# Kernel optimization log

Hardware: AMD Instinct MI355X
Metric: run time of the kernel (lower is better)

The kernel has to match this reference:

```python
import jax, jax.numpy as jnp
import numpy as np

N, F_IN, H, MH = 50000, 128, 128, 256
E = 800000

def _lin_init(key, out_d, in_d, bias=True):
    k1, k2 = jax.random.split(key)
    bound = 1.0 / np.sqrt(in_d)
    W = jax.random.uniform(k1, (out_d, in_d), minval=-bound, maxval=bound, dtype=jnp.float32)
    if bias:
        b = jax.random.uniform(k2, (out_d,), minval=-bound, maxval=bound, dtype=jnp.float32)
        return W, b
    return W, None

def setup_inputs() -> dict:
    key = jax.random.key(0)
    ks = jax.random.split(key, 8)
    x = jax.random.normal(ks[0], (N, F_IN), dtype=jnp.float32)
    edge_index = jax.random.randint(ks[1], (2, E), 0, N, dtype=jnp.int64)
    W1l, b1l = _lin_init(ks[2], H, F_IN, bias=True)   # SAGEConv1 neighbor lin (with bias)
    W1r, _ = _lin_init(ks[3], H, F_IN, bias=False)    # SAGEConv1 root lin (no bias)
    W2l, b2l = _lin_init(ks[4], H, H, bias=True)
    W2r, _ = _lin_init(ks[5], H, H, bias=False)
    Wm1, bm1 = _lin_init(ks[6], MH, 2 * H, bias=True)
    Wm2, bm2 = _lin_init(ks[7], 1, MH, bias=True)
    return {"x": x, "edge_index": edge_index,
            "W1l": W1l, "b1l": b1l, "W1r": W1r,
            "W2l": W2l, "b2l": b2l, "W2r": W2r,
            "Wm1": Wm1, "bm1": bm1, "Wm2": Wm2, "bm2": bm2}

def _sage_conv(x, src, dst, Wl, bl, Wr, num_nodes):
    # mean-aggregate messages x[src] at dst, then lin_l(agg) + lin_r(x)
    agg = jax.ops.segment_sum(x[src], dst, num_segments=num_nodes)
    cnt = jax.ops.segment_sum(jnp.ones((src.shape[0],), x.dtype), dst, num_segments=num_nodes)
    agg = agg / jnp.maximum(cnt, 1.0)[:, None]
    return agg @ Wl.T + bl + x @ Wr.T

def reference(x, edge_index, W1l, b1l, W1r, W2l, b2l, W2r, Wm1, bm1, Wm2, bm2):
    src, dst = edge_index[0], edge_index[1]
    n = x.shape[0]
    h = jax.nn.relu(_sage_conv(x, src, dst, W1l, b1l, W1r, n))
    # dropout is identity in eval mode
    h = jax.nn.relu(_sage_conv(h, src, dst, W2l, b2l, W2r, n))
    ef = jnp.concatenate([h[src], h[dst]], axis=-1)  # [E, 2H]
    out = jax.nn.relu(ef @ Wm1.T + bm1) @ Wm2.T + bm2
    return out.reshape(-1)
```

## Files before the change

### kernel.cpp

```cpp
#include <hip/hip_runtime.h>
#include <hip/hip_bf16.h>

#define NN 50000
#define F 128
#define EE 800000
#define MHD 256

typedef __attribute__((ext_vector_type(8))) short bf16x8;
typedef __attribute__((ext_vector_type(4))) float f32x4;

__device__ __forceinline__ float b2f(unsigned short u) {
    union { unsigned int i; float f; } v; v.i = ((unsigned)u) << 16; return v.f;
}
__device__ __forceinline__ unsigned short f2b(float f) {
    unsigned int x = __float_as_uint(f);
    unsigned int r = x + 0x7fffu + ((x >> 16) & 1u);
    return (unsigned short)(r >> 16);
}

__global__ __launch_bounds__(256) void cast_zero_kernel(
    const float* __restrict__ x,
    const float* __restrict__ W1l, const float* __restrict__ W1r,
    const float* __restrict__ W2l, const float* __restrict__ W2r,
    const float* __restrict__ Wm1,
    unsigned short* __restrict__ xb, unsigned short* __restrict__ wb,
    int* __restrict__ deg) {
    int bid = blockIdx.x;
    if (bid < 6250) {
        int i = (bid * 256 + threadIdx.x) * 4;
        float4 v = *(const float4*)(x + i);
        ushort4 o; o.x = f2b(v.x); o.y = f2b(v.y); o.z = f2b(v.z); o.w = f2b(v.w);
        *(ushort4*)(xb + i) = o;
    } else if (bid < 6378) {
        int i = ((bid - 6250) * 256 + threadIdx.x) * 4;
        unsigned short o[4];
        if (i < 32768) {
            const float* p = (i < 16384) ? (W1l + i) : (W1r + (i - 16384));
            float4 v = *(const float4*)p;
            o[0] = f2b(v.x); o[1] = f2b(v.y); o[2] = f2b(v.z); o[3] = f2b(v.w);
        } else if (i < 65536) {
            int local = i - 32768;
            const float* M = (local < 16384) ? W2l : W2r;
            int lm = local & 16383;
            int n = lm >> 7, kp = lm & 127;
#pragma unroll
            for (int t = 0; t < 4; t++) {
                int k = ((kp + t) & 7) * 16 + ((kp + t) >> 3);
                o[t] = f2b(M[n * 128 + k]);
            }
        } else {
            int local = i - 65536;
            int n = local >> 8, k2 = local & 255;
            int half = k2 >> 7, kp = k2 & 127;
#pragma unroll
            for (int t = 0; t < 4; t++) {
                int k = half * 128 + ((kp + t) & 7) * 16 + ((kp + t) >> 3);
                o[t] = f2b(Wm1[n * 256 + k]);
            }
        }
        *(ushort4*)(wb + i) = *(ushort4*)o;
    } else {
        int idx = ((bid - 6378) * 256 + threadIdx.x) * 4;
        if (idx < 50016) *(int4*)(deg + idx) = (int4){0, 0, 0, 0};
    }
}

__global__ __launch_bounds__(256) void edge_cvt_hist_kernel(
    const int* __restrict__ ei, int* __restrict__ s32, int* __restrict__ d32,
    int* __restrict__ deg) {
    __shared__ int isI64;
    if (threadIdx.x == 0) {
        int z = 0;
        for (int i = 1; i < 128; i += 2) z |= ei[i];
        isI64 = (z == 0) ? 1 : 0;
    }
    __syncthreads();
    int e = blockIdx.x * 256 + threadIdx.x;
    if (e >= EE) return;
    int s, d;
    if (isI64) {
        const long long* e64 = (const long long*)ei;
        s = (int)e64[e];
        d = (int)e64[EE + e];
    } else {
        s = ei[e];
        d = ei[EE + e];
    }
    s32[e] = s;
    d32[e] = d;
    atomicAdd(&deg[d], 1);
}

__global__ __launch_bounds__(1024) void scan_p1_kernel(
    const int* __restrict__ deg, int* __restrict__ exloc, int* __restrict__ bsum) {
    __shared__ int part[1024];
    int t = threadIdx.x, gid = blockIdx.x * 1024 + t;
    int v = (gid < NN) ? deg[gid] : 0;
    part[t] = v;
    __syncthreads();
    for (int off = 1; off < 1024; off <<= 1) {
        int u = (t >= off) ? part[t - off] : 0;
        __syncthreads();
        part[t] += u;
        __syncthreads();
    }
    exloc[gid] = part[t] - v;
    if (t == 1023) bsum[blockIdx.x] = part[t];
}

__global__ __launch_bounds__(1024) void scan_p3_kernel(
    const int* __restrict__ exloc, const int* __restrict__ bsum,
    int* __restrict__ rowstart, int* __restrict__ cursor) {
    __shared__ int offs;
    if (threadIdx.x == 0) {
        int s = 0;
        for (int b = 0; b < blockIdx.x; b++) s += bsum[b];
        offs = s;
    }
    __syncthreads();
    int gid = blockIdx.x * 1024 + threadIdx.x;
    if (gid > NN) return;
    if (gid == NN) { rowstart[NN] = EE; return; }
    int r = exloc[gid] + offs;
    rowstart[gid] = r;
    cursor[gid] = r;
}

__global__ __launch_bounds__(256) void fill_kernel(
    const int* __restrict__ s32, const int* __restrict__ d32,
    int* __restrict__ cursor, int2* __restrict__ nedge) {
    int e = blockIdx.x * 256 + threadIdx.x;
    if (e < EE) {
        int p = atomicAdd(&cursor[d32[e]], 1);
        nedge[p] = make_int2(s32[e], e);
    }
}

__global__ __launch_bounds__(256) void sage_layer_kernel(
    const unsigned short* __restrict__ xin,
    const int2* __restrict__ nedge, const int* __restrict__ rowstart,
    const unsigned short* __restrict__ W1, const unsigned short* __restrict__ W2,
    const float* __restrict__ bias,
    unsigned short* __restrict__ out) {
    __shared__ unsigned short lds[4][16][136];
    int wave = threadIdx.x >> 6, lane = threadIdx.x & 63;
    int m0 = (blockIdx.x * 4 + wave) * 16;

    int g = lane >> 4, l16 = lane & 15, col8 = l16 * 8;
    for (int batch = 0; batch < 4; batch++) {
        int node = m0 + batch * 4 + g;
        int beg = 0, end = 0;
        if (node < NN) { beg = rowstart[node]; end = rowstart[node + 1]; }
        float a[8] = {0,0,0,0,0,0,0,0};
        float b[8] = {0,0,0,0,0,0,0,0};
        int j = beg;
        for (; j + 7 < end; j += 8) {
            int s0 = nedge[j].x,     s1 = nedge[j + 1].x, s2 = nedge[j + 2].x, s3 = nedge[j + 3].x;
            int s4 = nedge[j + 4].x, s5 = nedge[j + 5].x, s6 = nedge[j + 6].x, s7 = nedge[j + 7].x;
            bf16x8 v0 = *(const bf16x8*)(xin + (size_t)s0 * F + col8);
            bf16x8 v1 = *(const bf16x8*)(xin + (size_t)s1 * F + col8);
            bf16x8 v2 = *(const bf16x8*)(xin + (size_t)s2 * F + col8);
            bf16x8 v3 = *(const bf16x8*)(xin + (size_t)s3 * F + col8);
            bf16x8 v4 = *(const bf16x8*)(xin + (size_t)s4 * F + col8);
            bf16x8 v5 = *(const bf16x8*)(xin + (size_t)s5 * F + col8);
            bf16x8 v6 = *(const bf16x8*)(xin + (size_t)s6 * F + col8);
            bf16x8 v7 = *(const bf16x8*)(xin + (size_t)s7 * F + col8);
            for (int i = 0; i < 8; i++)
                a[i] += (b2f((unsigned short)v0[i]) + b2f((unsigned short)v1[i]))
                      + (b2f((unsigned short)v2[i]) + b2f((unsigned short)v3[i]));
            for (int i = 0; i < 8; i++)
                b[i] += (b2f((unsigned short)v4[i]) + b2f((unsigned short)v5[i]))
                      + (b2f((unsigned short)v6[i]) + b2f((unsigned short)v7[i]));
        }
        for (; j + 3 < end; j += 4) {
            int s0 = nedge[j].x, s1 = nedge[j + 1].x, s2 = nedge[j + 2].x, s3 = nedge[j + 3].x;
            bf16x8 v0 = *(const bf16x8*)(xin + (size_t)s0 * F + col8);
            bf16x8 v1 = *(const bf16x8*)(xin + (size_t)s1 * F + col8);
            bf16x8 v2 = *(const bf16x8*)(xin + (size_t)s2 * F + col8);
            bf16x8 v3 = *(const bf16x8*)(xin + (size_t)s3 * F + col8);
            for (int i = 0; i < 8; i++)
                a[i] += (b2f((unsigned short)v0[i]) + b2f((unsigned short)v1[i]))
                      + (b2f((unsigned short)v2[i]) + b2f((unsigned short)v3[i]));
        }
        for (; j < end; j++) {
            int s0 = nedge[j].x;
            bf16x8 v0 = *(const bf16x8*)(xin + (size_t)s0 * F + col8);
            for (int i = 0; i < 8; i++) a[i] += b2f((unsigned short)v0[i]);
        }
        float inv = 1.0f / fmaxf((float)(end - beg), 1.0f);
        unsigned short o[8];
        for (int i = 0; i < 8; i++) o[i] = f2b((a[i] + b[i]) * inv);
        *(bf16x8*)&lds[wave][batch * 4 + g][col8] = *(bf16x8*)o;
    }
    __syncthreads();

    int c = lane & 15, q = lane >> 4;
    f32x4 acc[8];
    for (int nt = 0; nt < 8; nt++) {
        float b = bias[nt * 16 + c];
        acc[nt] = (f32x4){b, b, b, b};
    }
    int mrow = m0 + c; if (mrow > NN - 1) mrow = NN - 1;
    for (int op = 0; op < 2; op++) {
        const unsigned short* W = op ? W2 : W1;
        for (int kb = 0; kb < 4; kb++) {
            bf16x8 a;
            if (op == 0) a = *(const bf16x8*)&lds[wave][c][kb * 32 + q * 8];
            else         a = *(const bf16x8*)(xin + (size_t)mrow * F + kb * 32 + q * 8);
            for (int nt = 0; nt < 8; nt++) {
                bf16x8 b = *(const bf16x8*)(W + (size_t)(nt * 16 + c) * F + kb * 32 + q * 8);
                acc[nt] = __builtin_amdgcn_mfma_f32_16x16x32_bf16(a, b, acc[nt], 0, 0, 0);
            }
        }
    }
#pragma unroll
    for (int r = 0; r < 4; r++) {
        int node = m0 + q * 4 + r;
        if (node < NN) {
            unsigned short o[8];
#pragma unroll
            for (int nt = 0; nt < 8; nt++) o[nt] = f2b(fmaxf(acc[nt][r], 0.0f));
            *(bf16x8*)(out + (size_t)node * F + c * 8) = *(bf16x8*)o;
        }
    }
}

__global__ __launch_bounds__(256) void pq_gemm_kernel(
    const unsigned short* __restrict__ h,
    const unsigned short* __restrict__ wmb,
    const float* __restrict__ bm1,
    unsigned short* __restrict__ PQ) {
    int wave = threadIdx.x >> 6, lane = threadIdx.x & 63;
    int c = lane & 15, q = lane >> 4;
    int half = wave >> 1, ntBase = (wave & 1) * 8;
    int m0 = blockIdx.x * 16;
    int mrow = m0 + c; if (mrow > NN - 1) mrow = NN - 1;
    bf16x8 a[4];
#pragma unroll
    for (int kb = 0; kb < 4; kb++)
        a[kb] = *(const bf16x8*)(h + (size_t)mrow * F + kb * 32 + q * 8);
    f32x4 acc[8];
#pragma unroll
    for (int nt = 0; nt < 8; nt++) {
        float b = half ? bm1[(ntBase + nt) * 16 + c] : 0.0f;
        acc[nt] = (f32x4){b, b, b, b};
    }
#pragma unroll
    for (int kb = 0; kb < 4; kb++) {
#pragma unroll
        for (int nt = 0; nt < 8; nt++) {
            bf16x8 b = *(const bf16x8*)(wmb + (size_t)((ntBase + nt) * 16 + c) * 256 + half * 128 + kb * 32 + q * 8);
            acc[nt] = __builtin_amdgcn_mfma_f32_16x16x32_bf16(a[kb], b, acc[nt], 0, 0, 0);
        }
    }
#pragma unroll
    for (int r = 0; r < 4; r++) {
        int node = m0 + q * 4 + r;
        if (node < NN) {
            unsigned short o[8];
#pragma unroll
            for (int nt = 0; nt < 8; nt++) o[nt] = f2b(acc[nt][r]);
            *(bf16x8*)(PQ + (size_t)node * 512 + half * 256 + c * 16 + ntBase) = *(bf16x8*)o;
        }
    }
}

__global__ __launch_bounds__(256) void edge_dot_kernel(
    const unsigned short* __restrict__ PQ,
    const int2* __restrict__ nedge, const int* __restrict__ rowstart,
    const float* __restrict__ Wm2, const float* __restrict__ bm2,
    float* __restrict__ out) {
    int wave = threadIdx.x >> 6, lane = threadIdx.x & 63;
    int node = blockIdx.x * 4 + wave;
    if (node >= NN) return;
    int g = lane >> 4, l16 = lane & 15;
    int col = l16 * 16;
    float w2f[16], qf[16];
#pragma unroll
    for (int i = 0; i < 16; i++) w2f[i] = Wm2[i * 16 + l16];
    {
        bf16x8 q0 = *(const bf16x8*)(PQ + (size_t)node * 512 + 256 + col);
        bf16x8 q1 = *(const bf16x8*)(PQ + (size_t)node * 512 + 256 + col + 8);
#pragma unroll
        for (int i = 0; i < 8; i++) { qf[i] = b2f((unsigned short)q0[i]); qf[8 + i] = b2f((unsigned short)q1[i]); }
    }
    float b2 = bm2[0];
    int beg = rowstart[node], end = rowstart[node + 1];
    int j = beg + g;
    for (; j + 4 < end; j += 8) {
        int2 e0 = nedge[j], e1 = nedge[j + 4];
        uint4 a0 = *(const uint4*)(PQ + (size_t)e0.x * 512 + col);
        uint4 a1 = *(const uint4*)(PQ + (size_t)e0.x * 512 + col + 8);
        uint4 c0 = *(const uint4*)(PQ + (size_t)e1.x * 512 + col);
        uint4 c1 = *(const uint4*)(PQ + (size_t)e1.x * 512 + col + 8);
        float t0 = 0.f, t1 = 0.f;
        unsigned int w0[8] = {a0.x, a0.y, a0.z, a0.w, a1.x, a1.y, a1.z, a1.w};
        unsigned int w1[8] = {c0.x, c0.y, c0.z, c0.w, c1.x, c1.y, c1.z, c1.w};
#pragma unroll
        for (int i = 0; i < 8; i++) {
            float lo0 = __uint_as_float(w0[i] << 16);
            float hi0 = __uint_as_float(w0[i] & 0xffff0000u);
            float lo1 = __uint_as_float(w1[i] << 16);
            float hi1 = __uint_as_float(w1[i] & 0xffff0000u);
            t0 += fmaxf(lo0 + qf[2 * i], 0.f) * w2f[2 * i]
                + fmaxf(hi0 + qf[2 * i + 1], 0.f) * w2f[2 * i + 1];
            t1 += fmaxf(lo1 + qf[2 * i], 0.f) * w2f[2 * i]
                + fmaxf(hi1 + qf[2 * i + 1], 0.f) * w2f[2 * i + 1];
        }
        t0 += __shfl_xor(t0, 1);  t1 += __shfl_xor(t1, 1);
        t0 += __shfl_xor(t0, 2);  t1 += __shfl_xor(t1, 2);
        t0 += __shfl_xor(t0, 4);  t1 += __shfl_xor(t1, 4);
        t0 += __shfl_xor(t0, 8);  t1 += __shfl_xor(t1, 8);
        if (l16 == 0) { out[e0.y] = t0 + b2; out[e1.y] = t1 + b2; }
    }
    for (; j < end; j += 4) {
        int2 e0 = nedge[j];
        uint4 a0 = *(const uint4*)(PQ + (size_t)e0.x * 512 + col);
        uint4 a1 = *(const uint4*)(PQ + (size_t)e0.x * 512 + col + 8);
        unsigned int w0[8] = {a0.x, a0.y, a0.z, a0.w, a1.x, a1.y, a1.z, a1.w};
        float t = 0.f;
#pragma unroll
        for (int i = 0; i < 8; i++) {
            float lo = __uint_as_float(w0[i] << 16);
            float hi = __uint_as_float(w0[i] & 0xffff0000u);
            t += fmaxf(lo + qf[2 * i], 0.f) * w2f[2 * i]
               + fmaxf(hi + qf[2 * i + 1], 0.f) * w2f[2 * i + 1];
        }
        t += __shfl_xor(t, 1);
        t += __shfl_xor(t, 2);
        t += __shfl_xor(t, 4);
        t += __shfl_xor(t, 8);
        if (l16 == 0) out[e0.y] = t + b2;
    }
}

extern "C" void kernel_launch(void* const* d_in, const int* in_sizes, int n_in,
                              void* d_out, int out_size, void* d_ws, size_t ws_size,
                              hipStream_t stream) {
    const float* x   = (const float*)d_in[0];
    const int*   ei  = (const int*)d_in[1];
    const float* W1l = (const float*)d_in[2];
    const float* b1l = (const float*)d_in[3];
    const float* W1r = (const float*)d_in[4];
    const float* W2l = (const float*)d_in[5];
    const float* b2l = (const float*)d_in[6];
    const float* W2r = (const float*)d_in[7];
    const float* Wm1 = (const float*)d_in[8];
    const float* bm1 = (const float*)d_in[9];
    const float* Wm2 = (const float*)d_in[10];
    const float* bm2 = (const float*)d_in[11];

    char* ws = (char*)d_ws;
    unsigned short* PQ       = (unsigned short*)(ws);
    unsigned short* xb       = (unsigned short*)(ws);
    unsigned short* h1       = (unsigned short*)(ws + 12800000);
    unsigned short* wb       = (unsigned short*)(ws + 51200000);
    int*            s32      = (int*)(ws + 51462144);
    int*            d32      = (int*)(ws + 54662144);
    int*            deg      = (int*)(ws + 57862144);
    int*            rowstart = (int*)(ws + 58062208);
    int*            cursor   = (int*)(ws + 58262272);
    int2*           nedge    = (int2*)(ws + 58462336);
    unsigned short* h2       = (unsigned short*)(ws + 64862336);
    int*            exloc    = (int*)(ws + 77662336);
    int*            bsum     = (int*)(ws + 77867136);
    float*          outp     = (float*)d_out;

    const unsigned short* w1l_b  = wb;
    const unsigned short* w1r_b  = wb + 16384;
    const unsigned short* w2l_p  = wb + 32768;
    const unsigned short* w2r_p  = wb + 49152;
    const unsigned short* wm1_p  = wb + 65536;

    cast_zero_kernel<<<6427, 256, 0, stream>>>(x, W1l, W1r, W2l, W2r, Wm1, xb, wb, deg);
    edge_cvt_hist_kernel<<<3125, 256, 0, stream>>>(ei, s32, d32, deg);
    scan_p1_kernel<<<50, 1024, 0, stream>>>(deg, exloc, bsum);
    scan_p3_kernel<<<50, 1024, 0, stream>>>(exloc, bsum, rowstart, cursor);
    fill_kernel<<<3125, 256, 0, stream>>>(s32, d32, cursor, nedge);

    sage_layer_kernel<<<782, 256, 0, stream>>>(xb, nedge, rowstart, w1l_b, w1r_b, b1l, h1);
    sage_layer_kernel<<<782, 256, 0, stream>>>(h1, nedge, rowstart, w2l_p, w2r_p, b2l, h2);
    pq_gemm_kernel<<<3125, 256, 0, stream>>>(h2, wm1_p, bm1, PQ);
    edge_dot_kernel<<<12500, 256, 0, stream>>>(PQ, nedge, rowstart, Wm2, bm2, outp);
}
```

Before: 427.3 us.

## Make edge MLP kernel edge-parallel with packed src/dst indices

```diff
diff --git a/kernel.cpp b/kernel.cpp
--- a/kernel.cpp
+++ b/kernel.cpp
@@ -22,9 +22,9 @@
     const float* __restrict__ x,
     const float* __restrict__ W1l, const float* __restrict__ W1r,
     const float* __restrict__ W2l, const float* __restrict__ W2r,
-    const float* __restrict__ Wm1,
+    const float* __restrict__ Wm1, const float* __restrict__ Wm2,
     unsigned short* __restrict__ xb, unsigned short* __restrict__ wb,
-    int* __restrict__ deg) {
+    int* __restrict__ deg, float* __restrict__ w2p) {
     int bid = blockIdx.x;
     if (bid < 6250) {
         int i = (bid * 256 + threadIdx.x) * 4;
@@ -59,9 +59,12 @@
             }
         }
         *(ushort4*)(wb + i) = *(ushort4*)o;
-    } else {
+    } else if (bid < 6427) {
         int idx = ((bid - 6378) * 256 + threadIdx.x) * 4;
         if (idx < 50016) *(int4*)(deg + idx) = (int4){0, 0, 0, 0};
+    } else {
+        int t = threadIdx.x;
+        w2p[t] = Wm2[(t & 15) * 16 + (t >> 4)];
     }
 }
 
@@ -131,8 +134,9 @@
     int* __restrict__ cursor, int2* __restrict__ nedge) {
     int e = blockIdx.x * 256 + threadIdx.x;
     if (e < EE) {
-        int p = atomicAdd(&cursor[d32[e]], 1);
-        nedge[p] = make_int2(s32[e], e);
+        int d = d32[e];
+        int p = atomicAdd(&cursor[d], 1);
+        nedge[p] = make_int2((int)((unsigned)s32[e] | ((unsigned)d << 16)), e);
     }
 }
 
@@ -155,8 +159,10 @@
         float b[8] = {0,0,0,0,0,0,0,0};
         int j = beg;
         for (; j + 7 < end; j += 8) {
-            int s0 = nedge[j].x,     s1 = nedge[j + 1].x, s2 = nedge[j + 2].x, s3 = nedge[j + 3].x;
-            int s4 = nedge[j + 4].x, s5 = nedge[j + 5].x, s6 = nedge[j + 6].x, s7 = nedge[j + 7].x;
+            int s0 = nedge[j].x & 0xffff,     s1 = nedge[j + 1].x & 0xffff;
+            int s2 = nedge[j + 2].x & 0xffff, s3 = nedge[j + 3].x & 0xffff;
+            int s4 = nedge[j + 4].x & 0xffff, s5 = nedge[j + 5].x & 0xffff;
+            int s6 = nedge[j + 6].x & 0xffff, s7 = nedge[j + 7].x & 0xffff;
             bf16x8 v0 = *(const bf16x8*)(xin + (size_t)s0 * F + col8);
             bf16x8 v1 = *(const bf16x8*)(xin + (size_t)s1 * F + col8);
             bf16x8 v2 = *(const bf16x8*)(xin + (size_t)s2 * F + col8);
@@ -173,7 +179,8 @@
                       + (b2f((unsigned short)v6[i]) + b2f((unsigned short)v7[i]));
         }
         for (; j + 3 < end; j += 4) {
-            int s0 = nedge[j].x, s1 = nedge[j + 1].x, s2 = nedge[j + 2].x, s3 = nedge[j + 3].x;
+            int s0 = nedge[j].x & 0xffff,     s1 = nedge[j + 1].x & 0xffff;
+            int s2 = nedge[j + 2].x & 0xffff, s3 = nedge[j + 3].x & 0xffff;
             bf16x8 v0 = *(const bf16x8*)(xin + (size_t)s0 * F + col8);
             bf16x8 v1 = *(const bf16x8*)(xin + (size_t)s1 * F + col8);
             bf16x8 v2 = *(const bf16x8*)(xin + (size_t)s2 * F + col8);
@@ -183,7 +190,7 @@
                       + (b2f((unsigned short)v2[i]) + b2f((unsigned short)v3[i]));
         }
         for (; j < end; j++) {
-            int s0 = nedge[j].x;
+            int s0 = nedge[j].x & 0xffff;
             bf16x8 v0 = *(const bf16x8*)(xin + (size_t)s0 * F + col8);
             for (int i = 0; i < 8; i++) a[i] += b2f((unsigned short)v0[i]);
         }
@@ -267,70 +274,64 @@
 
 __global__ __launch_bounds__(256) void edge_dot_kernel(
     const unsigned short* __restrict__ PQ,
-    const int2* __restrict__ nedge, const int* __restrict__ rowstart,
-    const float* __restrict__ Wm2, const float* __restrict__ bm2,
+    const int2* __restrict__ nedge,
+    const float* __restrict__ w2p, const float* __restrict__ bm2,
     float* __restrict__ out) {
-    int wave = threadIdx.x >> 6, lane = threadIdx.x & 63;
-    int node = blockIdx.x * 4 + wave;
-    if (node >= NN) return;
-    int g = lane >> 4, l16 = lane & 15;
+    int t = threadIdx.x;
+    int l16 = t & 15;
+    int slot = t >> 4;
+    int p0 = blockIdx.x * 64 + slot * 4;
     int col = l16 * 16;
-    float w2f[16], qf[16];
-#pragma unroll
-    for (int i = 0; i < 16; i++) w2f[i] = Wm2[i * 16 + l16];
-    {
-        bf16x8 q0 = *(const bf16x8*)(PQ + (size_t)node * 512 + 256 + col);
-        bf16x8 q1 = *(const bf16x8*)(PQ + (size_t)node * 512 + 256 + col + 8);
-#pragma unroll
-        for (int i = 0; i < 8; i++) { qf[i] = b2f((unsigned short)q0[i]); qf[8 + i] = b2f((unsigned short)q1[i]); }
-    }
+    float w2f[16];
+    *(float4*)(w2f + 0)  = *(const float4*)(w2p + col + 0);
+    *(float4*)(w2f + 4)  = *(const float4*)(w2p + col + 4);
+    *(float4*)(w2f + 8)  = *(const float4*)(w2p + col + 8);
+    *(float4*)(w2f + 12) = *(const float4*)(w2p + col + 12);
     float b2 = bm2[0];
-    int beg = rowstart[node], end = rowstart[node + 1];
-    int j = beg + g;
-    for (; j + 4 < end; j += 8) {
-        int2 e0 = nedge[j], e1 = nedge[j + 4];
-        uint4 a0 = *(const uint4*)(PQ + (size_t)e0.x * 512 + col);
-        uint4 a1 = *(const uint4*)(PQ + (size_t)e0.x * 512 + col + 8);
-        uint4 c0 = *(const uint4*)(PQ + (size_t)e1.x * 512 + col);
-        uint4 c1 = *(const uint4*)(PQ + (size_t)e1.x * 512 + col + 8);
+#pragma unroll
+    for (int it = 0; it < 2; it++) {
+        int p = p0 + it * 2;
+        int2 e0 = nedge[p], e1 = nedge[p + 1];
+        unsigned v0 = (unsigned)e0.x, v1 = (unsigned)e1.x;
+        int s0 = (int)(v0 & 0xffffu), d0 = (int)(v0 >> 16);
+        int s1 = (int)(v1 & 0xffffu), d1 = (int)(v1 >> 16);
+        const unsigned short* P0 = PQ + (size_t)s0 * 512 + col;
+        const unsigned short* Q0 = PQ + (size_t)d0 * 512 + 256 + col;
+        const unsigned short* P1 = PQ + (size_t)s1 * 512 + col;
+        const unsigned short* Q1 = PQ + (size_t)d1 * 512 + 256 + col;
+        uint4 pa = *(const uint4*)(P0);
+        uint4 pb = *(const uint4*)(P0 + 8);
+        uint4 qa = *(const uint4*)(Q0);
+        uint4 qb = *(const uint4*)(Q0 + 8);
+        uint4 pc = *(const uint4*)(P1);
+        uint4 pd = *(const uint4*)(P1 + 8);
+        uint4 qc = *(const uint4*)(Q1);
+        uint4 qd = *(const uint4*)(Q1 + 8);
+        unsigned int wp0[8] = {pa.x, pa.y, pa.z, pa.w, pb.x, pb.y, pb.z, pb.w};
+        unsigned int wq0[8] = {qa.x, qa.y, qa.z, qa.w, qb.x, qb.y, qb.z, qb.w};
+        unsigned int wp1[8] = {pc.x, pc.y, pc.z, pc.w, pd.x, pd.y, pd.z, pd.w};
+        unsigned int wq1[8] = {qc.x, qc.y, qc.z, qc.w, qd.x, qd.y, qd.z, qd.w};
         float t0 = 0.f, t1 = 0.f;
-        unsigned int w0[8] = {a0.x, a0.y, a0.z, a0.w, a1.x, a1.y, a1.z, a1.w};
-        unsigned int w1[8] = {c0.x, c0.y, c0.z, c0.w, c1.x, c1.y, c1.z, c1.w};
 #pragma unroll
         for (int i = 0; i < 8; i++) {
-            float lo0 = __uint_as_float(w0[i] << 16);
-            float hi0 = __uint_as_float(w0[i] & 0xffff0000u);
-            float lo1 = __uint_as_float(w1[i] << 16);
-            float hi1 = __uint_as_float(w1[i] & 0xffff0000u);
-            t0 += fmaxf(lo0 + qf[2 * i], 0.f) * w2f[2 * i]
-                + fmaxf(hi0 + qf[2 * i + 1], 0.f) * w2f[2 * i + 1];
-            t1 += fmaxf(lo1 + qf[2 * i], 0.f) * w2f[2 * i]
-                + fmaxf(hi1 + qf[2 * i + 1], 0.f) * w2f[2 * i + 1];
+            float plo0 = __uint_as_float(wp0[i] << 16);
+            float phi0 = __uint_as_float(wp0[i] & 0xffff0000u);
+            float qlo0 = __uint_as_float(wq0[i] << 16);
+            float qhi0 = __uint_as_float(wq0[i] & 0xffff0000u);
+            t0 += fmaxf(plo0 + qlo0, 0.f) * w2f[2 * i]
+                + fmaxf(phi0 + qhi0, 0.f) * w2f[2 * i + 1];
+            float plo1 = __uint_as_float(wp1[i] << 16);
+            float phi1 = __uint_as_float(wp1[i] & 0xffff0000u);
+            float qlo1 = __uint_as_float(wq1[i] << 16);
+            float qhi1 = __uint_as_float(wq1[i] & 0xffff0000u);
+            t1 += fmaxf(plo1 + qlo1, 0.f) * w2f[2 * i]
+                + fmaxf(phi1 + qhi1, 0.f) * w2f[2 * i + 1];
         }
         t0 += __shfl_xor(t0, 1);  t1 += __shfl_xor(t1, 1);
         t0 += __shfl_xor(t0, 2);  t1 += __shfl_xor(t1, 2);
         t0 += __shfl_xor(t0, 4);  t1 += __shfl_xor(t1, 4);
         t0 += __shfl_xor(t0, 8);  t1 += __shfl_xor(t1, 8);
         if (l16 == 0) { out[e0.y] = t0 + b2; out[e1.y] = t1 + b2; }
-    }
-    for (; j < end; j += 4) {
-        int2 e0 = nedge[j];
-        uint4 a0 = *(const uint4*)(PQ + (size_t)e0.x * 512 + col);
-        uint4 a1 = *(const uint4*)(PQ + (size_t)e0.x * 512 + col + 8);
-        unsigned int w0[8] = {a0.x, a0.y, a0.z, a0.w, a1.x, a1.y, a1.z, a1.w};
-        float t = 0.f;
-#pragma unroll
-        for (int i = 0; i < 8; i++) {
-            float lo = __uint_as_float(w0[i] << 16);
-            float hi = __uint_as_float(w0[i] & 0xffff0000u);
-            t += fmaxf(lo + qf[2 * i], 0.f) * w2f[2 * i]
-               + fmaxf(hi + qf[2 * i + 1], 0.f) * w2f[2 * i + 1];
-        }
-        t += __shfl_xor(t, 1);
-        t += __shfl_xor(t, 2);
-        t += __shfl_xor(t, 4);
-        t += __shfl_xor(t, 8);
-        if (l16 == 0) out[e0.y] = t + b2;
     }
 }
 
@@ -364,6 +365,7 @@
     unsigned short* h2       = (unsigned short*)(ws + 64862336);
     int*            exloc    = (int*)(ws + 77662336);
     int*            bsum     = (int*)(ws + 77867136);
+    float*          w2p      = (float*)(ws + 77868032);
     float*          outp     = (float*)d_out;
 
     const unsigned short* w1l_b  = wb;
@@ -372,7 +374,7 @@
     const unsigned short* w2r_p  = wb + 49152;
     const unsigned short* wm1_p  = wb + 65536;
 
-    cast_zero_kernel<<<6427, 256, 0, stream>>>(x, W1l, W1r, W2l, W2r, Wm1, xb, wb, deg);
+    cast_zero_kernel<<<6428, 256, 0, stream>>>(x, W1l, W1r, W2l, W2r, Wm1, Wm2, xb, wb, deg, w2p);
     edge_cvt_hist_kernel<<<3125, 256, 0, stream>>>(ei, s32, d32, deg);
     scan_p1_kernel<<<50, 1024, 0, stream>>>(deg, exloc, bsum);
     scan_p3_kernel<<<50, 1024, 0, stream>>>(exloc, bsum, rowstart, cursor);
@@ -381,5 +383,5 @@
     sage_layer_kernel<<<782, 256, 0, stream>>>(xb, nedge, rowstart, w1l_b, w1r_b, b1l, h1);
     sage_layer_kernel<<<782, 256, 0, stream>>>(h1, nedge, rowstart, w2l_p, w2r_p, b2l, h2);
     pq_gemm_kernel<<<3125, 256, 0, stream>>>(h2, wm1_p, bm1, PQ);
-    edge_dot_kernel<<<12500, 256, 0, stream>>>(PQ, nedge, rowstart, Wm2, bm2, outp);
-}
+    edge_dot_kernel<<<12500, 256, 0, stream>>>(PQ, nedge, w2p, bm2, outp);
+}
```

New measurement: 424.2 us. Within noise of the previous version (-0.7%).
